# Kernel tuning notes

Measured on AMD Instinct MI355X. Metric: run time of the kernel, lower is better.

## Reference

```python
import jax, jax.numpy as jnp
import numpy as np

B, J, H, OUT_LEN = 16, 2048, 2048, 128  # seq_len J must equal hidden_dim H
HDIM = H // OUT_LEN  # 16


def setup_inputs() -> dict:
    key = jax.random.key(0)
    k_vec, k_wq, k_wk, k_wv = jax.random.split(key, 4)
    scale = 1.0 / np.sqrt(H)  # keep projections well-scaled (xavier-like)
    return {
        "vec": jax.random.normal(k_vec, (B, J, H), dtype=jnp.float32),
        "wq_w": jax.random.normal(k_wq, (OUT_LEN, H), dtype=jnp.float32) * scale,
        "wq_b": jnp.ones((OUT_LEN,), dtype=jnp.float32),
        "wk_w": jax.random.normal(k_wk, (H, H), dtype=jnp.float32) * scale,
        "wk_b": jnp.ones((H,), dtype=jnp.float32),
        "wv_w": jax.random.normal(k_wv, (HDIM, H), dtype=jnp.float32) * scale,
        "wv_b": jnp.ones((HDIM,), dtype=jnp.float32),
    }


def reference(vec, wq_w, wq_b, wk_w, wk_b, wv_w, wv_b):
    # Projections (nn.Linear: x @ W.T + b)
    q = vec @ wq_w.T + wq_b          # [B, J, out_len]
    k = vec @ wk_w.T + wk_b          # [B, J, H]
    v = vec @ wv_w.T + wv_b          # [B, J, hdim]
    # attn[b, i, h] = sum_j q[b, j, i] * k[b, j, h]  -> [B, out_len, H]
    attn = jnp.einsum('bji,bjk->bij', q, k)
    attn = jax.nn.softmax(jnp.tanh(attn), axis=-1)
    # ret[b, i, d] = sum_j attn[b, i, j] * v[b, j, d]  (requires H == J)
    ret = jnp.einsum('bij,bjk->bik', attn, v)  # [B, out_len, hdim]
    return ret
```

## Files before the change

### kernel.cpp

```cpp
#include <hip/hip_runtime.h>
#include <hip/hip_bf16.h>
#include <math.h>

#define Bn   16
#define Jn   2048
#define Hn   2048
#define OUTn 128
#define HDn  16

#define KC      64
#define NCHUNK  (Hn / KC)
#define A_UNITS 512
#define B_UNITS 1280
#define WPK_CHUNK_BYTES (2 * B_UNITS * 16)

#define WS_PART1 2048
#define WS_WPK   (WS_PART1 + 256 * 2048)
#define WS_PART  (WS_WPK + NCHUNK * 2 * B_UNITS * 4)

typedef __attribute__((ext_vector_type(8))) short bf16x8_t;
typedef __attribute__((ext_vector_type(4))) float f32x4_t;

typedef __attribute__((address_space(1))) const void gvoid_t;
typedef __attribute__((address_space(3))) void lvoid_t;

__device__ __forceinline__ unsigned short f2bf(float x) {
  unsigned u = __builtin_bit_cast(unsigned, x);
  unsigned r = (u + 0x7fffu + ((u >> 16) & 1u)) >> 16;
  return (unsigned short)r;
}
__device__ __forceinline__ float bf2f(unsigned short h) {
  unsigned u = ((unsigned)h) << 16;
  return __builtin_bit_cast(float, u);
}

__global__ __launch_bounds__(256) void prep1_kernel(const float* __restrict__ wk_w,
                                                    const float* __restrict__ wk_b,
                                                    float* __restrict__ ws) {
  const int blk = blockIdx.x;
  const int tid = threadIdx.x;
  if (blk < 256) {
    const int h0 = blk * 8;
    const int c0 = tid * 8;
    float a[8] = {0.f, 0.f, 0.f, 0.f, 0.f, 0.f, 0.f, 0.f};
#pragma unroll
    for (int h = 0; h < 8; ++h) {
      const float* row = wk_w + (size_t)(h0 + h) * Hn + c0;
      const float4 u = *(const float4*)row;
      const float4 v = *(const float4*)(row + 4);
      a[0] += u.x; a[1] += u.y; a[2] += u.z; a[3] += u.w;
      a[4] += v.x; a[5] += v.y; a[6] += v.z; a[7] += v.w;
    }
    float* dst = ws + WS_PART1 + (size_t)blk * Hn + c0;
    *(float4*)dst       = make_float4(a[0], a[1], a[2], a[3]);
    *(float4*)(dst + 4) = make_float4(a[4], a[5], a[6], a[7]);
  } else {
    __shared__ float red[256];
    float s = 0.f;
    for (int h = tid; h < Hn; h += 256) s += wk_b[h];
    red[tid] = s;
    __syncthreads();
    for (int off = 128; off > 0; off >>= 1) {
      if (tid < off) red[tid] += red[tid + off];
      __syncthreads();
    }
    if (tid == 0) ws[0] = red[0];
  }
}

__global__ __launch_bounds__(256) void prep2_kernel(const float* __restrict__ wq_w,
                                                    const float* __restrict__ wv_w,
                                                    const float* __restrict__ ws,
                                                    uint4* __restrict__ wpk) {
  const int id = blockIdx.x * 256 + threadIdx.x;
  const int chunk = id / B_UNITS;
  const int u     = id % B_UNITS;
  const int kblk  = u / 640;
  const int u2    = u % 640;
  const int nt    = u2 >> 6;
  const int g     = (u2 >> 4) & 3;
  const int n16   = u2 & 15;
  const int n     = nt * 16 + n16;
  const int k     = chunk * KC + kblk * 32 + g * 8;

  float x[8];
  if (n < OUTn) {
    const float* s = wq_w + (size_t)n * Hn + k;
#pragma unroll
    for (int i = 0; i < 8; ++i) x[i] = s[i];
  } else if (n < OUTn + HDn) {
    const float* s = wv_w + (size_t)(n - OUTn) * Hn + k;
#pragma unroll
    for (int i = 0; i < 8; ++i) x[i] = s[i];
  } else if (n == OUTn + HDn) {
#pragma unroll
    for (int i = 0; i < 8; ++i) x[i] = 0.f;
    const float* p1 = ws + WS_PART1 + k;
    for (int p = 0; p < 256; ++p) {
      const float4 a = *(const float4*)p1;
      const float4 b = *(const float4*)(p1 + 4);
      x[0] += a.x; x[1] += a.y; x[2] += a.z; x[3] += a.w;
      x[4] += b.x; x[5] += b.y; x[6] += b.z; x[7] += b.w;
      p1 += Hn;
    }
  } else {
#pragma unroll
    for (int i = 0; i < 8; ++i) x[i] = 0.f;
  }

  unsigned short hi[8], lo[8];
#pragma unroll
  for (int i = 0; i < 8; ++i) {
    hi[i] = f2bf(x[i]);
    lo[i] = f2bf(x[i] - bf2f(hi[i]));
  }
  uint4 uh, ul;
  uh.x = (unsigned)hi[0] | ((unsigned)hi[1] << 16);
  uh.y = (unsigned)hi[2] | ((unsigned)hi[3] << 16);
  uh.z = (unsigned)hi[4] | ((unsigned)hi[5] << 16);
  uh.w = (unsigned)hi[6] | ((unsigned)hi[7] << 16);
  ul.x = (unsigned)lo[0] | ((unsigned)lo[1] << 16);
  ul.y = (unsigned)lo[2] | ((unsigned)lo[3] << 16);
  ul.z = (unsigned)lo[4] | ((unsigned)lo[5] << 16);
  ul.w = (unsigned)lo[6] | ((unsigned)lo[7] << 16);
  wpk[(size_t)(chunk * 2 + 0) * B_UNITS + u] = uh;
  wpk[(size_t)(chunk * 2 + 1) * B_UNITS + u] = ul;
}

__global__ __launch_bounds__(256, 2) void proj_kernel(
    const float* __restrict__ vec,
    const float* __restrict__ wq_b,
    const float* __restrict__ wv_b,
    const float* __restrict__ wsc,
    const uint4* __restrict__ wpk,
    float* __restrict__ part)
{
  __shared__ uint4 As[2 * A_UNITS];
  __shared__ uint4 Bs[2 * B_UNITS];

  const int tid   = threadIdx.x;
  const int lane  = tid & 63;
  const int w     = tid >> 6;
  const int wm    = w >> 1;
  const int wn    = w & 1;
  const int b     = blockIdx.x >> 5;
  const int jt    = blockIdx.x & 31;
  const int j0    = jt * 64;
  const int col16 = lane & 15;
  const int rbase = (lane >> 4) * 4;

  const float* vecb = vec + (size_t)b * Jn * Hn;
  const bf16x8_t* As8 = (const bf16x8_t*)As;
  const bf16x8_t* Bs8 = (const bf16x8_t*)Bs;

  f32x4_t acc[2][5];
#pragma unroll
  for (int mi = 0; mi < 2; ++mi)
#pragma unroll
    for (int ni = 0; ni < 5; ++ni) acc[mi][ni] = (f32x4_t){0.f, 0.f, 0.f, 0.f};

  for (int chunk = 0; chunk < NCHUNK; ++chunk) {
    const int k0 = chunk * KC;
#pragma unroll
    for (int rep = 0; rep < 2; ++rep) {
      const int u    = tid + rep * 256;
      const int kblk = u >> 8;
      const int mt   = (u >> 6) & 3;
      const int g    = (u >> 4) & 3;
      const int m    = u & 15;
      const float* src = vecb + (size_t)(j0 + mt * 16 + m) * Hn + k0 + kblk * 32 + g * 8;
      const float4 a0 = *(const float4*)src;
      const float4 a1 = *(const float4*)(src + 4);
      float x[8] = {a0.x, a0.y, a0.z, a0.w, a1.x, a1.y, a1.z, a1.w};
      unsigned short hi[8], lo[8];
#pragma unroll
      for (int i = 0; i < 8; ++i) {
        hi[i] = f2bf(x[i]);
        lo[i] = f2bf(x[i] - bf2f(hi[i]));
      }
      uint4 uh, ul;
      uh.x = (unsigned)hi[0] | ((unsigned)hi[1] << 16);
      uh.y = (unsigned)hi[2] | ((unsigned)hi[3] << 16);
      uh.z = (unsigned)hi[4] | ((unsigned)hi[5] << 16);
      uh.w = (unsigned)hi[6] | ((unsigned)hi[7] << 16);
      ul.x = (unsigned)lo[0] | ((unsigned)lo[1] << 16);
      ul.y = (unsigned)lo[2] | ((unsigned)lo[3] << 16);
      ul.z = (unsigned)lo[4] | ((unsigned)lo[5] << 16);
      ul.w = (unsigned)lo[6] | ((unsigned)lo[7] << 16);
      As[u]           = uh;
      As[A_UNITS + u] = ul;
    }
    {
      const char* gbase = (const char*)wpk + (size_t)chunk * WPK_CHUNK_BYTES + (size_t)lane * 16;
#pragma unroll
      for (int i = 0; i < 10; ++i) {
        const int q = w + i * 4;
        __builtin_amdgcn_global_load_lds((gvoid_t*)(gbase + q * 1024),
                                         (lvoid_t*)&Bs[q * 64], 16, 0, 0);
      }
    }
    __syncthreads();

#pragma unroll
    for (int kblk = 0; kblk < 2; ++kblk) {
      bf16x8_t bh[5], bl[5];
#pragma unroll
      for (int ni = 0; ni < 5; ++ni) {
        const int idx = (kblk * 10 + wn * 5 + ni) * 64 + lane;
        bh[ni] = Bs8[idx];
        bl[ni] = Bs8[B_UNITS + idx];
      }
#pragma unroll
      for (int mi = 0; mi < 2; ++mi) {
        const int aidx = (kblk * 4 + wm * 2 + mi) * 64 + lane;
        const bf16x8_t ah = As8[aidx];
        const bf16x8_t al = As8[A_UNITS + aidx];
#pragma unroll
        for (int ni = 0; ni < 5; ++ni) {
          acc[mi][ni] = __builtin_amdgcn_mfma_f32_16x16x32_bf16(ah, bh[ni], acc[mi][ni], 0, 0, 0);
          acc[mi][ni] = __builtin_amdgcn_mfma_f32_16x16x32_bf16(ah, bl[ni], acc[mi][ni], 0, 0, 0);
          acc[mi][ni] = __builtin_amdgcn_mfma_f32_16x16x32_bf16(al, bh[ni], acc[mi][ni], 0, 0, 0);
        }
      }
    }
    __syncthreads();
  }

  const float wkb = wsc[0];
  float* ks_s = (float*)&As[0];
  float* vt   = ks_s + 64;
  float* epi  = (float*)&Bs[0];

  if (wn == 1) {
    const float vb_ = wv_b[col16];
#pragma unroll
    for (int mi = 0; mi < 2; ++mi) {
      const f32x4_t c = acc[mi][3];
#pragma unroll
      for (int r = 0; r < 4; ++r) {
        const int j = (wm * 2 + mi) * 16 + rbase + r;
        vt[j * 20 + col16] = c[r] + vb_;
      }
    }
    if (col16 == 0) {
#pragma unroll
      for (int mi = 0; mi < 2; ++mi) {
        const f32x4_t c = acc[mi][4];
#pragma unroll
        for (int r = 0; r < 4; ++r) {
          const int j = (wm * 2 + mi) * 16 + rbase + r;
          ks_s[j] = c[r] + wkb;
        }
      }
    }
  }
  __syncthreads();

  const int NCOL = wn ? 3 : 5;
  float* epiw = epi + wm * 128 * 18;

#pragma unroll 5
  for (int ni = 0; ni < 5; ++ni) {
    if (ni < NCOL) {
      const float qb = wq_b[(wn * 5 + ni) * 16 + col16];
      float pz = 0.f;
      float po[16];
#pragma unroll
      for (int d = 0; d < 16; ++d) po[d] = 0.f;
#pragma unroll
      for (int mi = 0; mi < 2; ++mi) {
#pragma unroll
        for (int r = 0; r < 4; ++r) {
          const int j = (wm * 2 + mi) * 16 + rbase + r;
          const float ksj = ks_s[j];
          const float4 v0 = *(const float4*)&vt[j * 20];
          const float4 v1 = *(const float4*)&vt[j * 20 + 4];
          const float4 v2 = *(const float4*)&vt[j * 20 + 8];
          const float4 v3 = *(const float4*)&vt[j * 20 + 12];
          const float q   = acc[mi][ni][r] + qb;
          const float e2x = __expf(2.f * q * ksj);
          const float t   = 1.f - 2.f / (e2x + 1.f);
          const float p   = __expf(t);
          pz += p;
          po[0]  += p * v0.x; po[1]  += p * v0.y; po[2]  += p * v0.z; po[3]  += p * v0.w;
          po[4]  += p * v1.x; po[5]  += p * v1.y; po[6]  += p * v1.z; po[7]  += p * v1.w;
          po[8]  += p * v2.x; po[9]  += p * v2.y; po[10] += p * v2.z; po[11] += p * v2.w;
          po[12] += p * v3.x; po[13] += p * v3.y; po[14] += p * v3.z; po[15] += p * v3.w;
        }
      }
      pz += __shfl_xor(pz, 16);
      pz += __shfl_xor(pz, 32);
#pragma unroll
      for (int d = 0; d < 16; ++d) {
        po[d] += __shfl_xor(po[d], 16);
        po[d] += __shfl_xor(po[d], 32);
      }
      if (lane < 16) {
        const int n = (wn * 5 + ni) * 16 + lane;
        epiw[n * 18 + 16] = pz;
#pragma unroll
        for (int d = 0; d < 16; ++d) epiw[n * 18 + d] = po[d];
      }
    }
  }
  __syncthreads();
  float* pout = part + ((size_t)(b * 32 + jt) * 128) * 17;
  for (int idx = tid; idx < 128 * 17; idx += 256) {
    const int row = idx / 17, c = idx % 17;
    pout[idx] = epi[row * 18 + c] + epi[128 * 18 + row * 18 + c];
  }
}

__global__ __launch_bounds__(256) void finalize_kernel(const float* __restrict__ part,
                                                       float* __restrict__ out) {
  const int gid = blockIdx.x * 256 + threadIdx.x;
  const float* p = part + (size_t)(gid >> 7) * 32 * 128 * 17 + (size_t)(gid & 127) * 17;
  float z = 0.f;
  float o[16];
#pragma unroll
  for (int d = 0; d < 16; ++d) o[d] = 0.f;
  for (int jt = 0; jt < 32; ++jt) {
    const float* pp = p + (size_t)jt * 128 * 17;
    z += pp[16];
#pragma unroll
    for (int d = 0; d < 16; ++d) o[d] += pp[d];
  }
  const float inv = 1.f / z;
  float* dst = out + (size_t)gid * 16;
#pragma unroll
  for (int d = 0; d < 16; ++d) dst[d] = o[d] * inv;
}

extern "C" void kernel_launch(void* const* d_in, const int* in_sizes, int n_in,
                              void* d_out, int out_size, void* d_ws, size_t ws_size,
                              hipStream_t stream) {
  const float* vec  = (const float*)d_in[0];
  const float* wq_w = (const float*)d_in[1];
  const float* wq_b = (const float*)d_in[2];
  const float* wk_w = (const float*)d_in[3];
  const float* wk_b = (const float*)d_in[4];
  const float* wv_w = (const float*)d_in[5];
  const float* wv_b = (const float*)d_in[6];

  float* ws   = (float*)d_ws;
  uint4* wpk  = (uint4*)(ws + WS_WPK);
  float* part = ws + WS_PART;
  float* out  = (float*)d_out;

  prep1_kernel<<<257, 256, 0, stream>>>(wk_w, wk_b, ws);
  prep2_kernel<<<(NCHUNK * B_UNITS) / 256, 256, 0, stream>>>(wq_w, wv_w, ws, wpk);
  proj_kernel<<<Bn * (Jn / 64), 256, 0, stream>>>(vec, wq_b, wv_b, ws, wpk, part);
  finalize_kernel<<<8, 256, 0, stream>>>(part, out);
}
```

Measured before the change: 451.5 us.

## Double-buffer weight tiles in LDS and feed A operand directly from registers

Restructures the projection GEMM main loop so the packed weights are double-buffered in LDS via async global-to-LDS loads, prefetching the next chunk while the current one computes, with one barrier per chunk instead of two. The vec activations are no longer staged in LDS. Each wave loads its own 16 rows straight into registers in the MFMA fragment layout, converts them to hi/lo bf16 and keeps them prefetched one chunk ahead. Each wave now covers all 10 N-tiles for its 16 rows, so the epilogue has to route q through LDS. The change also adds unroll pragmas to the prep and finalize loops, and it risks more register pressure and relies on a hand-placed vmcnt wait.

```diff
diff --git a/kernel.cpp b/kernel.cpp
--- a/kernel.cpp
+++ b/kernel.cpp
@@ -10,7 +10,6 @@
 
 #define KC      64
 #define NCHUNK  (Hn / KC)
-#define A_UNITS 512
 #define B_UNITS 1280
 #define WPK_CHUNK_BYTES (2 * B_UNITS * 16)
 
@@ -32,6 +31,17 @@
 __device__ __forceinline__ float bf2f(unsigned short h) {
   unsigned u = ((unsigned)h) << 16;
   return __builtin_bit_cast(float, u);
+}
+
+__device__ __forceinline__ void cvt8(const float4 u, const float4 v,
+                                     bf16x8_t& h, bf16x8_t& l) {
+  float x[8] = {u.x, u.y, u.z, u.w, v.x, v.y, v.z, v.w};
+#pragma unroll
+  for (int i = 0; i < 8; ++i) {
+    const unsigned short hi = f2bf(x[i]);
+    h[i] = (short)hi;
+    l[i] = (short)f2bf(x[i] - bf2f(hi));
+  }
 }
 
 __global__ __launch_bounds__(256) void prep1_kernel(const float* __restrict__ wk_w,
@@ -96,6 +106,7 @@
 #pragma unroll
     for (int i = 0; i < 8; ++i) x[i] = 0.f;
     const float* p1 = ws + WS_PART1 + k;
+#pragma unroll 8
     for (int p = 0; p < 256; ++p) {
       const float4 a = *(const float4*)p1;
       const float4 b = *(const float4*)(p1 + 4);
@@ -135,127 +146,119 @@
     const uint4* __restrict__ wpk,
     float* __restrict__ part)
 {
-  __shared__ uint4 As[2 * A_UNITS];
-  __shared__ uint4 Bs[2 * B_UNITS];
+  __shared__ uint4 Bs[2][2 * B_UNITS];
 
   const int tid   = threadIdx.x;
   const int lane  = tid & 63;
   const int w     = tid >> 6;
-  const int wm    = w >> 1;
-  const int wn    = w & 1;
   const int b     = blockIdx.x >> 5;
   const int jt    = blockIdx.x & 31;
   const int j0    = jt * 64;
   const int col16 = lane & 15;
   const int rbase = (lane >> 4) * 4;
 
-  const float* vecb = vec + (size_t)b * Jn * Hn;
-  const bf16x8_t* As8 = (const bf16x8_t*)As;
-  const bf16x8_t* Bs8 = (const bf16x8_t*)Bs;
-
-  f32x4_t acc[2][5];
-#pragma unroll
-  for (int mi = 0; mi < 2; ++mi)
-#pragma unroll
-    for (int ni = 0; ni < 5; ++ni) acc[mi][ni] = (f32x4_t){0.f, 0.f, 0.f, 0.f};
-
-  for (int chunk = 0; chunk < NCHUNK; ++chunk) {
-    const int k0 = chunk * KC;
-#pragma unroll
-    for (int rep = 0; rep < 2; ++rep) {
-      const int u    = tid + rep * 256;
-      const int kblk = u >> 8;
-      const int mt   = (u >> 6) & 3;
-      const int g    = (u >> 4) & 3;
-      const int m    = u & 15;
-      const float* src = vecb + (size_t)(j0 + mt * 16 + m) * Hn + k0 + kblk * 32 + g * 8;
-      const float4 a0 = *(const float4*)src;
-      const float4 a1 = *(const float4*)(src + 4);
-      float x[8] = {a0.x, a0.y, a0.z, a0.w, a1.x, a1.y, a1.z, a1.w};
-      unsigned short hi[8], lo[8];
-#pragma unroll
-      for (int i = 0; i < 8; ++i) {
-        hi[i] = f2bf(x[i]);
-        lo[i] = f2bf(x[i] - bf2f(hi[i]));
-      }
-      uint4 uh, ul;
-      uh.x = (unsigned)hi[0] | ((unsigned)hi[1] << 16);
-      uh.y = (unsigned)hi[2] | ((unsigned)hi[3] << 16);
-      uh.z = (unsigned)hi[4] | ((unsigned)hi[5] << 16);
-      uh.w = (unsigned)hi[6] | ((unsigned)hi[7] << 16);
-      ul.x = (unsigned)lo[0] | ((unsigned)lo[1] << 16);
-      ul.y = (unsigned)lo[2] | ((unsigned)lo[3] << 16);
-      ul.z = (unsigned)lo[4] | ((unsigned)lo[5] << 16);
-      ul.w = (unsigned)lo[6] | ((unsigned)lo[7] << 16);
-      As[u]           = uh;
-      As[A_UNITS + u] = ul;
-    }
-    {
-      const char* gbase = (const char*)wpk + (size_t)chunk * WPK_CHUNK_BYTES + (size_t)lane * 16;
-#pragma unroll
-      for (int i = 0; i < 10; ++i) {
-        const int q = w + i * 4;
-        __builtin_amdgcn_global_load_lds((gvoid_t*)(gbase + q * 1024),
-                                         (lvoid_t*)&Bs[q * 64], 16, 0, 0);
-      }
-    }
-    __syncthreads();
-
-#pragma unroll
-    for (int kblk = 0; kblk < 2; ++kblk) {
-      bf16x8_t bh[5], bl[5];
-#pragma unroll
-      for (int ni = 0; ni < 5; ++ni) {
-        const int idx = (kblk * 10 + wn * 5 + ni) * 64 + lane;
-        bh[ni] = Bs8[idx];
-        bl[ni] = Bs8[B_UNITS + idx];
-      }
-#pragma unroll
-      for (int mi = 0; mi < 2; ++mi) {
-        const int aidx = (kblk * 4 + wm * 2 + mi) * 64 + lane;
-        const bf16x8_t ah = As8[aidx];
-        const bf16x8_t al = As8[A_UNITS + aidx];
-#pragma unroll
-        for (int ni = 0; ni < 5; ++ni) {
-          acc[mi][ni] = __builtin_amdgcn_mfma_f32_16x16x32_bf16(ah, bh[ni], acc[mi][ni], 0, 0, 0);
-          acc[mi][ni] = __builtin_amdgcn_mfma_f32_16x16x32_bf16(ah, bl[ni], acc[mi][ni], 0, 0, 0);
-          acc[mi][ni] = __builtin_amdgcn_mfma_f32_16x16x32_bf16(al, bh[ni], acc[mi][ni], 0, 0, 0);
-        }
-      }
-    }
-    __syncthreads();
-  }
+  const float* aptr = vec + (size_t)b * Jn * Hn
+                    + (size_t)(j0 + w * 16 + col16) * Hn + (lane >> 4) * 8;
+
+  f32x4_t acc[10];
+#pragma unroll
+  for (int ni = 0; ni < 10; ++ni) acc[ni] = (f32x4_t){0.f, 0.f, 0.f, 0.f};
+
+#define STAGE_B(ch_, buf_)                                                    \
+  do {                                                                        \
+    const char* gb_ = (const char*)wpk + (size_t)(ch_) * WPK_CHUNK_BYTES +    \
+                      (size_t)lane * 16;                                      \
+    uint4* bd_ = &Bs[buf_][0];                                                \
+    _Pragma("unroll")                                                         \
+    for (int i_ = 0; i_ < 10; ++i_) {                                         \
+      const int q_ = w + i_ * 4;                                              \
+      __builtin_amdgcn_global_load_lds((gvoid_t*)(gb_ + q_ * 1024),           \
+                                       (lvoid_t*)(bd_ + q_ * 64), 16, 0, 0);  \
+    }                                                                         \
+  } while (0)
+
+#define CHUNK_BODY(ch_, buf_, u0, u1, u2, u3, v0_, v1_, v2_, v3_)             \
+  do {                                                                        \
+    if ((ch_) + 1 < NCHUNK) { STAGE_B((ch_) + 1, (buf_) ^ 1); }               \
+    asm volatile("" ::: "memory");     \
+    if ((ch_) + 1 < NCHUNK) {                                                 \
+      const float* ap_ = aptr + (size_t)((ch_) + 1) * KC;                     \
+      v0_ = *(const float4*)(ap_);                                            \
+      v1_ = *(const float4*)(ap_ + 4);                                        \
+      v2_ = *(const float4*)(ap_ + 32);                                       \
+      v3_ = *(const float4*)(ap_ + 36);                                       \
+    }                                                                         \
+    bf16x8_t ah0_, al0_, ah1_, al1_;                                          \
+    cvt8(u0, u1, ah0_, al0_);                                                 \
+    cvt8(u2, u3, ah1_, al1_);                                                 \
+    const bf16x8_t* B8_ = (const bf16x8_t*)&Bs[buf_][0];                      \
+    _Pragma("unroll")                                                         \
+    for (int kb_ = 0; kb_ < 2; ++kb_) {                                       \
+      const bf16x8_t ah_ = kb_ ? ah1_ : ah0_;                                 \
+      const bf16x8_t al_ = kb_ ? al1_ : al0_;                                 \
+      _Pragma("unroll")                                                       \
+      for (int ni_ = 0; ni_ < 10; ++ni_) {                                    \
+        const int idx_ = (kb_ * 10 + ni_) * 64 + lane;                        \
+        const bf16x8_t bh_ = B8_[idx_];                                       \
+        const bf16x8_t bl_ = B8_[B_UNITS + idx_];                             \
+        acc[ni_] = __builtin_amdgcn_mfma_f32_16x16x32_bf16(ah_, bh_, acc[ni_], 0, 0, 0); \
+        acc[ni_] = __builtin_amdgcn_mfma_f32_16x16x32_bf16(ah_, bl_, acc[ni_], 0, 0, 0); \
+        acc[ni_] = __builtin_amdgcn_mfma_f32_16x16x32_bf16(al_, bh_, acc[ni_], 0, 0, 0); \
+      }                                                                       \
+    }                                                                         \
+    asm volatile("s_waitcnt vmcnt(4)" ::: "memory");  \
+    __builtin_amdgcn_s_barrier();                                             \
+  } while (0)
+
+  STAGE_B(0, 0);
+  asm volatile("" ::: "memory");
+  float4 c0 = *(const float4*)(aptr);
+  float4 c1 = *(const float4*)(aptr + 4);
+  float4 c2 = *(const float4*)(aptr + 32);
+  float4 c3 = *(const float4*)(aptr + 36);
+  asm volatile("s_waitcnt vmcnt(4)" ::: "memory");
+  __builtin_amdgcn_s_barrier();
+
+  float4 n0, n1, n2, n3;
+  for (int ch = 0; ch < NCHUNK; ch += 2) {
+    CHUNK_BODY(ch,     0, c0, c1, c2, c3, n0, n1, n2, n3);
+    CHUNK_BODY(ch + 1, 1, n0, n1, n2, n3, c0, c1, c2, c3);
+  }
+#undef CHUNK_BODY
+#undef STAGE_B
 
   const float wkb = wsc[0];
-  float* ks_s = (float*)&As[0];
-  float* vt   = ks_s + 64;
-  float* epi  = (float*)&Bs[0];
-
-  if (wn == 1) {
+  float* q_lds = (float*)Bs;
+  float* ks_s  = q_lds + 64 * 132;
+  float* vt    = ks_s + 64;
+  float* epi   = vt + 64 * 20;
+
+  {
+#pragma unroll
+    for (int ni = 0; ni < 8; ++ni) {
+#pragma unroll
+      for (int r = 0; r < 4; ++r) {
+        q_lds[(size_t)(w * 16 + rbase + r) * 132 + ni * 16 + col16] = acc[ni][r];
+      }
+    }
     const float vb_ = wv_b[col16];
 #pragma unroll
-    for (int mi = 0; mi < 2; ++mi) {
-      const f32x4_t c = acc[mi][3];
+    for (int r = 0; r < 4; ++r) {
+      const int jj = w * 16 + rbase + r;
+      vt[jj * 20 + col16] = acc[8][r] + vb_;
+    }
+    if (col16 == 0) {
 #pragma unroll
       for (int r = 0; r < 4; ++r) {
-        const int j = (wm * 2 + mi) * 16 + rbase + r;
-        vt[j * 20 + col16] = c[r] + vb_;
-      }
-    }
-    if (col16 == 0) {
-#pragma unroll
-      for (int mi = 0; mi < 2; ++mi) {
-        const f32x4_t c = acc[mi][4];
-#pragma unroll
-        for (int r = 0; r < 4; ++r) {
-          const int j = (wm * 2 + mi) * 16 + rbase + r;
-          ks_s[j] = c[r] + wkb;
-        }
+        const int jj = w * 16 + rbase + r;
+        ks_s[jj] = acc[9][r] + wkb;
       }
     }
   }
   __syncthreads();
 
+  const int wm   = w >> 1;
+  const int wn   = w & 1;
   const int NCOL = wn ? 3 : 5;
   float* epiw = epi + wm * 128 * 18;
 
@@ -277,7 +280,7 @@
           const float4 v1 = *(const float4*)&vt[j * 20 + 4];
           const float4 v2 = *(const float4*)&vt[j * 20 + 8];
           const float4 v3 = *(const float4*)&vt[j * 20 + 12];
-          const float q   = acc[mi][ni][r] + qb;
+          const float q   = q_lds[(size_t)j * 132 + (wn * 5 + ni) * 16 + col16] + qb;
           const float e2x = __expf(2.f * q * ksj);
           const float t   = 1.f - 2.f / (e2x + 1.f);
           const float p   = __expf(t);
@@ -319,6 +322,7 @@
   float o[16];
 #pragma unroll
   for (int d = 0; d < 16; ++d) o[d] = 0.f;
+#pragma unroll 4
   for (int jt = 0; jt < 32; ++jt) {
     const float* pp = p + (size_t)jt * 128 * 17;
     z += pp[16];
```

New measurement: 449.0 us. Within noise of the previous version (-0.5%).
